# Kernel optimization log

Measured on AMD Instinct MI355X. Metric: run time of the kernel, lower is better.

The kernel has to match this reference:

```python
import jax, jax.numpy as jnp
import numpy as np

B, C, H, W = 8, 512, 64, 64
RED = 4
CR = C // RED  # 128

def setup_inputs() -> dict:
    key = jax.random.key(0)
    k1, k2, k3 = jax.random.split(key, 3)
    x = jax.random.normal(k1, (B, C, H, W), dtype=jnp.float32)
    # conv_in: 1x1 conv, no bias -> weight [3*CR, C]
    w_in = jax.random.normal(k2, (3 * CR, C), dtype=jnp.float32) * 0.02
    # conv_out: 1x1 conv, no bias -> weight [C, CR]
    w_out = jax.random.normal(k3, (C, CR), dtype=jnp.float32) * 0.02
    return {"x": x, "w_in": w_in, "w_out": w_out}

def reference(x, w_in, w_out):
    b, c, h, w = x.shape
    n = h * w
    xf = x.reshape(b, c, n)                         # flatten spatial -> [B,C,N]
    proj = jnp.einsum('oc,bcn->bon', w_in, xf)      # 1x1 conv_in -> [B,3*CR,N]
    emb_a, emb_b, g = jnp.split(proj, 3, axis=1)    # each [B,CR,N]
    # unscaled full self-attention over N spatial tokens
    weights = jnp.einsum('bcn,bcm->bnm', emb_a, emb_b)   # [B,N,N]
    weights = jax.nn.softmax(weights, axis=2)
    y = jnp.einsum('bnm,bcm->bnc', weights, g)           # [B,N,CR]
    y = jnp.einsum('oc,bnc->bon', w_out, y)              # 1x1 conv_out -> [B,C,N]
    return x + y.reshape(b, c, h, w)
```

## Files before the change

kernel.cpp:

```cpp
#include <hip/hip_runtime.h>


typedef __attribute__((ext_vector_type(8))) short short8;
typedef __attribute__((ext_vector_type(4))) float f32x4;
typedef __attribute__((ext_vector_type(16))) float f32x16;
typedef __attribute__((ext_vector_type(2))) unsigned int uint2v;

__device__ inline unsigned bfr(float f) {
  union { float f; unsigned u; } v; v.f = f;
  return v.u + 0x8000u;
}
__device__ inline unsigned short f2bf(float f) { return (unsigned short)(bfr(f) >> 16); }
__device__ inline unsigned pack2(float a, float b) {
  return __builtin_amdgcn_perm(bfr(b), bfr(a), 0x07060302u);
}
__device__ inline unsigned cvtpk(float a, float b) {
  unsigned r;
  asm("v_cvt_pk_bf16_f32 %0, %1, %2" : "=v"(r) : "v"(a), "v"(b));
  return r;
}
__device__ inline int sw(int row, int col, int stride_halves) {
  return row * stride_halves + ((((col >> 3) ^ (row & 7)) << 3) | (col & 7));
}
__device__ inline void load_lds16(const void* g, void* l) {
  __builtin_amdgcn_global_load_lds(
      (const __attribute__((address_space(1))) unsigned int*)g,
      (__attribute__((address_space(3))) unsigned int*)l, 16, 0, 0);
}

__global__ __launch_bounds__(256) void k_prep(const float* __restrict__ w_in,
                                              const float* __restrict__ w_out,
                                              unsigned short* __restrict__ wi,
                                              unsigned short* __restrict__ wo) {
  int i = blockIdx.x * 256 + threadIdx.x;
  const float* src;
  unsigned short* dst;
  int base;
  float s = 1.0f;
  if (i < 24576) {
    src = w_in;  dst = wi; base = i * 8;
    if (base < 128 * 512) s = 1.4426950408889634f;
  } else {
    src = w_out; dst = wo; base = (i - 24576) * 8;
  }
  float4 d0 = *(const float4*)&src[base];
  float4 d1 = *(const float4*)&src[base + 4];
  d0.x *= s; d0.y *= s; d0.z *= s; d0.w *= s;
  d1.x *= s; d1.y *= s; d1.z *= s; d1.w *= s;
  uint4 p;
  p.x = pack2(d0.x, d0.y); p.y = pack2(d0.z, d0.w);
  p.z = pack2(d1.x, d1.y); p.w = pack2(d1.z, d1.w);
  *(uint4*)&dst[base] = p;
}

__global__ __launch_bounds__(256, 2) void k_proj(const float* __restrict__ x,
                                                 const unsigned short* __restrict__ wi,
                                                 unsigned short* __restrict__ ab,
                                                 unsigned short* __restrict__ gC) {
  __shared__ unsigned short A_lds[384 * 64];
  __shared__ unsigned short B_lds[64 * 64];
  const int t = threadIdx.x;
  const int lane = t & 63;
  const int w = t >> 6;
  const int l15 = lane & 15;
  const int quad = lane >> 4;
  const int n0 = blockIdx.x * 64;
  const int b = blockIdx.y;
  const int ch8g = t >> 5;
  const int tp = t & 31;

  f32x4 acc[6][4];
#pragma unroll
  for (int i = 0; i < 6; i++)
#pragma unroll
    for (int j = 0; j < 4; j++) acc[i][j] = (f32x4)0.f;

  float2 d[8];
#pragma unroll
  for (int j = 0; j < 8; j++)
    d[j] = *(const float2*)&x[((size_t)(b * 512 + ch8g * 8 + j)) * 4096 + n0 + tp * 2];

  for (int k0 = 0; k0 < 512; k0 += 64) {
#pragma unroll
    for (int j = 0; j < 12; j++) {
      int row = w * 96 + j * 8 + (lane >> 3);
      int gs = (lane & 7) ^ (row & 7);
      load_lds16(&wi[(size_t)row * 512 + k0 + gs * 8],
                 (void*)&A_lds[(w * 96 + j * 8) * 64]);
    }
#pragma unroll
    for (int i = 0; i < 2; i++) {
      int r = tp * 2 + i;
      uint4 pv;
      if (i == 0) {
        pv.x = pack2(d[0].x, d[1].x); pv.y = pack2(d[2].x, d[3].x);
        pv.z = pack2(d[4].x, d[5].x); pv.w = pack2(d[6].x, d[7].x);
      } else {
        pv.x = pack2(d[0].y, d[1].y); pv.y = pack2(d[2].y, d[3].y);
        pv.z = pack2(d[4].y, d[5].y); pv.w = pack2(d[6].y, d[7].y);
      }
      *(uint4*)&B_lds[sw(r, ch8g * 8, 64)] = pv;
    }
    if (k0 + 64 < 512) {
#pragma unroll
      for (int j = 0; j < 8; j++)
        d[j] = *(const float2*)&x[((size_t)(b * 512 + k0 + 64 + ch8g * 8 + j)) * 4096 + n0 + tp * 2];
    }
    __syncthreads();
#pragma unroll
    for (int kk = 0; kk < 64; kk += 32) {
      short8 a[6];
#pragma unroll
      for (int m = 0; m < 6; m++)
        a[m] = *(const short8*)&A_lds[sw(w * 96 + m * 16 + l15, kk + quad * 8, 64)];
#pragma unroll
      for (int ns = 0; ns < 4; ns++) {
        short8 bb = *(const short8*)&B_lds[sw(ns * 16 + l15, kk + quad * 8, 64)];
#pragma unroll
        for (int m = 0; m < 6; m++)
          acc[m][ns] = __builtin_amdgcn_mfma_f32_16x16x32_bf16(a[m], bb, acc[m][ns], 0, 0, 0);
      }
    }
    __syncthreads();
  }
#pragma unroll
  for (int m = 0; m < 6; m++) {
    int o = w * 96 + m * 16 + quad * 4;
    if (o < 256) {
#pragma unroll
      for (int ns = 0; ns < 4; ns++) {
        int n = n0 + ns * 16 + l15;
        uint2 p;
        p.x = pack2(acc[m][ns][0], acc[m][ns][1]);
        p.y = pack2(acc[m][ns][2], acc[m][ns][3]);
        *(uint2*)&ab[((size_t)(b * 4096 + n)) * 256 + o] = p;
      }
    } else {
      int og = o - 256;
#pragma unroll
      for (int ns = 0; ns < 4; ns++) {
        int n = n0 + ns * 16 + l15;
#pragma unroll
        for (int r = 0; r < 4; r++)
          gC[((size_t)(b * 128 + og + r)) * 4096 + n] = f2bf(acc[m][ns][r]);
      }
    }
  }
}

__global__ __launch_bounds__(512, 2) void k_attn(const unsigned short* __restrict__ ab,
                                                 const unsigned short* __restrict__ gC,
                                                 unsigned short* __restrict__ yt) {
  __shared__ uint4 smem4[65536 / 16];
  unsigned short* smem_h = (unsigned short*)smem4;
  float* Obuf = (float*)smem4;
  float* lsumbuf = (float*)((char*)smem4 + 33024);
  unsigned* Pbuf = (unsigned*)((char*)smem4 + 33280);

  const int t = threadIdx.x;
  const int lane = t & 63;
  const int w = t >> 6;
  const int wr = w & 1;
  const int wc = w >> 1;
  const int l31 = lane & 31;
  const int h = lane >> 5;
  const int b = blockIdx.x & 7;
  const int q0 = (blockIdx.x >> 3) * 128;

  short8 qf[8];
  {
    const unsigned short* qp = &ab[((size_t)(b * 4096 + q0 + wc * 32 + l31)) * 256 + h * 8];
#pragma unroll
    for (int ks = 0; ks < 8; ks++) qf[ks] = *(const short8*)&qp[ks * 16];
  }

  auto dma_tile = [&](int kt, int buf) {
    unsigned short* Kb = smem_h + buf * 8192;
    unsigned short* Vb = smem_h + 16384 + buf * 8192;
#pragma unroll
    for (int j = 0; j < 2; j++) {
      int ck = w * 2 + j;
      int wrc = ck >> 3, ksc = ck & 7;
      load_lds16(&ab[((size_t)(b * 4096 + kt + wrc * 32 + l31)) * 256 + 128 + ksc * 16 + h * 8],
                 (void*)&Kb[ck * 512]);
    }
#pragma unroll
    for (int j = 0; j < 2; j++) {
      int cv = w * 2 + j;
      int ctc = cv >> 2, wrc = (cv >> 1) & 1, fc = cv & 1;
      load_lds16(&gC[((size_t)(b * 128 + ctc * 32 + l31)) * 4096 + kt + (wrc * 4 + fc * 2 + h) * 8],
                 (void*)&Vb[cv * 512]);
    }
  };

  f32x16 O[4];
#pragma unroll
  for (int i = 0; i < 4; i++) O[i] = (f32x16)0.f;
  float ls0 = 0.f, ls1 = 0.f, ls2 = 0.f, ls3 = 0.f;

  dma_tile(0, 0);
  __syncthreads();

  for (int it = 0; it < 64; ++it) {
    if (it < 63) dma_tile((it + 1) * 64, (it + 1) & 1);
    const unsigned short* Kc = smem_h + (it & 1) * 8192;
    const unsigned short* Vc = smem_h + 16384 + (it & 1) * 8192;

    f32x16 accS = (f32x16)0.f;
    __builtin_amdgcn_s_setprio(1);
#pragma unroll
    for (int ks = 0; ks < 8; ks++) {
      short8 ak = *(const short8*)&Kc[(wr * 8 + ks) * 512 + lane * 8];
      accS = __builtin_amdgcn_mfma_f32_32x32x16_bf16(ak, qf[ks], accS, 0, 0, 0);
    }
    __builtin_amdgcn_s_setprio(0);

    float ps[16];
#pragma unroll
    for (int r = 0; r < 16; r++) ps[r] = __builtin_amdgcn_exp2f(accS[r]);
    ls0 += ps[0] + ps[4];  ls1 += ps[1] + ps[5];
    ls2 += ps[2] + ps[6];  ls3 += ps[3] + ps[7];
    ls0 += ps[8] + ps[12]; ls1 += ps[9] + ps[13];
    ls2 += ps[10] + ps[14]; ls3 += ps[11] + ps[15];
    unsigned u[8];
#pragma unroll
    for (int i = 0; i < 8; i++) u[i] = cvtpk(ps[2 * i], ps[2 * i + 1]);

    short8 pfrag[2];
#pragma unroll
    for (int f = 0; f < 2; f++) {
      uint2v r02 = __builtin_amdgcn_permlane32_swap(u[4 * f + 0], u[4 * f + 2], false, false);
      uint2v r13 = __builtin_amdgcn_permlane32_swap(u[4 * f + 1], u[4 * f + 3], false, false);
      union { unsigned uu[4]; short8 s; } cv;
      cv.uu[0] = r02[0]; cv.uu[1] = r13[0]; cv.uu[2] = r02[1]; cv.uu[3] = r13[1];
      pfrag[f] = cv.s;
    }

    __builtin_amdgcn_s_setprio(1);
#pragma unroll
    for (int ct = 0; ct < 4; ct++) {
#pragma unroll
      for (int f = 0; f < 2; f++) {
        short8 av = *(const short8*)&Vc[(ct * 4 + wr * 2 + f) * 512 + lane * 8];
        O[ct] = __builtin_amdgcn_mfma_f32_32x32x16_bf16(av, pfrag[f], O[ct], 0, 0, 0);
      }
    }
    __builtin_amdgcn_s_setprio(0);
    __syncthreads();
  }

  float lsum = (ls0 + ls1) + (ls2 + ls3);
  lsum += __shfl_xor(lsum, 32);
#pragma unroll
  for (int p = 0; p < 2; ++p) {
    const bool act = (wc >> 1) == p;
    const int q = (wc & 1) * 32 + l31;
    if (act && wr == 0) {
#pragma unroll
      for (int ct = 0; ct < 4; ct++)
#pragma unroll
        for (int r = 0; r < 16; r++) {
          int c = ct * 32 + (r & 3) + 8 * (r >> 2) + 4 * h;
          Obuf[q * 129 + c] = O[ct][r];
        }
      if (h == 0) lsumbuf[q] = lsum;
    }
    __syncthreads();
    if (act && wr == 1) {
      float linv = 1.f / (lsum + lsumbuf[q]);
#pragma unroll
      for (int ct = 0; ct < 4; ct++)
#pragma unroll
        for (int r = 0; r < 16; r += 2) {
          int c = ct * 32 + (r & 3) + 8 * (r >> 2) + 4 * h;
          float v0 = (Obuf[q * 129 + c] + O[ct][r]) * linv;
          float v1 = (Obuf[q * 129 + c + 1] + O[ct][r + 1]) * linv;
          Pbuf[q * 65 + (c >> 1)] = pack2(v0, v1);
        }
    }
    __syncthreads();
    {
      int qq = t >> 3, seg = t & 7;
      unsigned* yrow = (unsigned*)&yt[((size_t)(b * 4096 + q0 + p * 64 + qq)) * 128];
#pragma unroll
      for (int i = 0; i < 2; i++) {
        int base = qq * 65 + seg * 8 + i * 4;
        uint4 v;
        v.x = Pbuf[base + 0];
        v.y = Pbuf[base + 1];
        v.z = Pbuf[base + 2];
        v.w = Pbuf[base + 3];
        *(uint4*)&yrow[seg * 8 + i * 4] = v;
      }
    }
  }
}

__global__ __launch_bounds__(256) void k_out(const float* __restrict__ x,
                                             const unsigned short* __restrict__ wo,
                                             const unsigned short* __restrict__ yt,
                                             float* __restrict__ out) {
  __shared__ unsigned short A_lds[128 * 128];
  __shared__ unsigned short B_lds[64 * 128];
  const int t = threadIdx.x;
  const int lane = t & 63;
  const int w = t >> 6;
  const int l15 = lane & 15;
  const int quad = lane >> 4;
  const int id = blockIdx.x;
  const int b = id & 7;
  const int rest = id >> 3;
  const int o0 = (rest & 3) * 128;
  const int n0 = (rest >> 2) * 64;

#pragma unroll
  for (int j = 0; j < 8; j++) {
    int row = w * 32 + j * 4 + (lane >> 4);
    int gs = (lane & 15) ^ (row & 7);
    load_lds16(&wo[(size_t)(o0 + row) * 128 + gs * 8],
               (void*)&A_lds[(w * 32 + j * 4) * 128]);
  }
#pragma unroll
  for (int j = 0; j < 4; j++) {
    int row = w * 16 + j * 4 + (lane >> 4);
    int gs = (lane & 15) ^ (row & 7);
    load_lds16(&yt[((size_t)(b * 4096 + n0 + row)) * 128 + gs * 8],
               (void*)&B_lds[(w * 16 + j * 4) * 128]);
  }
  __syncthreads();

  f32x4 acc[2][4];
#pragma unroll
  for (int i = 0; i < 2; i++)
#pragma unroll
    for (int j = 0; j < 4; j++) acc[i][j] = (f32x4)0.f;
#pragma unroll
  for (int ks = 0; ks < 4; ks++) {
    short8 a0 = *(const short8*)&A_lds[sw(w * 32 + l15, ks * 32 + quad * 8, 128)];
    short8 a1 = *(const short8*)&A_lds[sw(w * 32 + 16 + l15, ks * 32 + quad * 8, 128)];
#pragma unroll
    for (int ns = 0; ns < 4; ns++) {
      short8 bb = *(const short8*)&B_lds[sw(ns * 16 + l15, ks * 32 + quad * 8, 128)];
      acc[0][ns] = __builtin_amdgcn_mfma_f32_16x16x32_bf16(a0, bb, acc[0][ns], 0, 0, 0);
      acc[1][ns] = __builtin_amdgcn_mfma_f32_16x16x32_bf16(a1, bb, acc[1][ns], 0, 0, 0);
    }
  }
#pragma unroll
  for (int ms = 0; ms < 2; ms++) {
    int o = o0 + w * 32 + ms * 16 + quad * 4;
#pragma unroll
    for (int ns = 0; ns < 4; ns++) {
      int n = n0 + ns * 16 + l15;
#pragma unroll
      for (int r = 0; r < 4; r++) {
        size_t off = ((size_t)(b * 512 + o + r)) * 4096 + n;
        out[off] = x[off] + acc[ms][ns][r];
      }
    }
  }
}

extern "C" void kernel_launch(void* const* d_in, const int* in_sizes, int n_in,
                              void* d_out, int out_size, void* d_ws, size_t ws_size,
                              hipStream_t stream) {
  const float* x = (const float*)d_in[0];
  const float* w_in = (const float*)d_in[1];
  const float* w_out = (const float*)d_in[2];
  float* out = (float*)d_out;

  unsigned short* ab = (unsigned short*)d_ws;
  unsigned short* gC = ab + (size_t)8 * 4096 * 256;
  unsigned short* yt = gC + (size_t)8 * 128 * 4096;
  unsigned short* wi = yt + (size_t)8 * 4096 * 128;
  unsigned short* wo = wi + (size_t)384 * 512;

  k_prep<<<128, 256, 0, stream>>>(w_in, w_out, wi, wo);
  k_proj<<<dim3(64, 8), 256, 0, stream>>>(x, wi, ab, gC);
  k_attn<<<dim3(256), 512, 0, stream>>>(ab, gC, yt);
  k_out<<<2048, 256, 0, stream>>>(x, wo, yt, out);
}
```

Baseline: 229.4 us.

## Store K and V projections in pre-tiled LDS layout for contiguous attention loads

The projection kernel now writes Q to its own compact buffer and writes K and V directly in the per-64-key tile layout that the attention kernel's LDS staging expects. The attention tile loads become fully contiguous 8KB-per-tile copies instead of strided gathers across rows and channels. The cost is more scattered stores in the projection kernel, particularly the per-element V writes.

```diff
diff --git a/kernel.cpp b/kernel.cpp
--- a/kernel.cpp
+++ b/kernel.cpp
@@ -55,8 +55,9 @@
 
 __global__ __launch_bounds__(256, 2) void k_proj(const float* __restrict__ x,
                                                  const unsigned short* __restrict__ wi,
-                                                 unsigned short* __restrict__ ab,
-                                                 unsigned short* __restrict__ gC) {
+                                                 unsigned short* __restrict__ aq,
+                                                 unsigned short* __restrict__ Kf,
+                                                 unsigned short* __restrict__ Vf) {
   __shared__ unsigned short A_lds[384 * 64];
   __shared__ unsigned short B_lds[64 * 64];
   const int t = threadIdx.x;
@@ -64,7 +65,8 @@
   const int w = t >> 6;
   const int l15 = lane & 15;
   const int quad = lane >> 4;
-  const int n0 = blockIdx.x * 64;
+  const int tl = blockIdx.x;
+  const int n0 = tl * 64;
   const int b = blockIdx.y;
   const int ch8g = t >> 5;
   const int tp = t & 31;
@@ -123,33 +125,53 @@
     }
     __syncthreads();
   }
+  const size_t tbase = ((size_t)(b * 64 + tl)) * 8192;
 #pragma unroll
   for (int m = 0; m < 6; m++) {
     int o = w * 96 + m * 16 + quad * 4;
-    if (o < 256) {
+    if (o < 128) {
 #pragma unroll
       for (int ns = 0; ns < 4; ns++) {
         int n = n0 + ns * 16 + l15;
         uint2 p;
         p.x = pack2(acc[m][ns][0], acc[m][ns][1]);
         p.y = pack2(acc[m][ns][2], acc[m][ns][3]);
-        *(uint2*)&ab[((size_t)(b * 4096 + n)) * 256 + o] = p;
+        *(uint2*)&aq[((size_t)(b * 4096 + n)) * 128 + o] = p;
+      }
+    } else if (o < 256) {
+      int c = o - 128;
+      int ksc = c >> 4, hk = (c >> 3) & 1, e0 = c & 7;
+#pragma unroll
+      for (int ns = 0; ns < 4; ns++) {
+        int key = ns * 16 + l15;
+        int ck = (key >> 5) * 8 + ksc;
+        int lane_k = hk * 32 + (key & 31);
+        uint2 p;
+        p.x = pack2(acc[m][ns][0], acc[m][ns][1]);
+        p.y = pack2(acc[m][ns][2], acc[m][ns][3]);
+        *(uint2*)&Kf[tbase + ck * 512 + lane_k * 8 + e0] = p;
       }
     } else {
-      int og = o - 256;
+      int cb = o - 256;
 #pragma unroll
       for (int ns = 0; ns < 4; ns++) {
-        int n = n0 + ns * 16 + l15;
-#pragma unroll
-        for (int r = 0; r < 4; r++)
-          gC[((size_t)(b * 128 + og + r)) * 4096 + n] = f2bf(acc[m][ns][r]);
-      }
-    }
-  }
-}
-
-__global__ __launch_bounds__(512, 2) void k_attn(const unsigned short* __restrict__ ab,
-                                                 const unsigned short* __restrict__ gC,
+        int key = ns * 16 + l15;
+        int g8 = key >> 3;
+        int e = key & 7;
+        size_t kb = tbase + (size_t)((g8 & 1) * 32) * 8 + e + (size_t)(g8 >> 1) * 512;
+#pragma unroll
+        for (int r = 0; r < 4; r++) {
+          int c = cb + r;
+          Vf[kb + (size_t)(c >> 5) * 4 * 512 + (size_t)(c & 31) * 8] = f2bf(acc[m][ns][r]);
+        }
+      }
+    }
+  }
+}
+
+__global__ __launch_bounds__(512, 2) void k_attn(const unsigned short* __restrict__ aq,
+                                                 const unsigned short* __restrict__ Kf,
+                                                 const unsigned short* __restrict__ Vf,
                                                  unsigned short* __restrict__ yt) {
   __shared__ uint4 smem4[65536 / 16];
   unsigned short* smem_h = (unsigned short*)smem4;
@@ -169,27 +191,21 @@
 
   short8 qf[8];
   {
-    const unsigned short* qp = &ab[((size_t)(b * 4096 + q0 + wc * 32 + l31)) * 256 + h * 8];
+    const unsigned short* qp = &aq[((size_t)(b * 4096 + q0 + wc * 32 + l31)) * 128 + h * 8];
 #pragma unroll
     for (int ks = 0; ks < 8; ks++) qf[ks] = *(const short8*)&qp[ks * 16];
   }
 
-  auto dma_tile = [&](int kt, int buf) {
+  auto dma_tile = [&](int tl, int buf) {
     unsigned short* Kb = smem_h + buf * 8192;
     unsigned short* Vb = smem_h + 16384 + buf * 8192;
+    const unsigned short* Ks = &Kf[((size_t)(b * 64 + tl)) * 8192];
+    const unsigned short* Vs = &Vf[((size_t)(b * 64 + tl)) * 8192];
 #pragma unroll
     for (int j = 0; j < 2; j++) {
       int ck = w * 2 + j;
-      int wrc = ck >> 3, ksc = ck & 7;
-      load_lds16(&ab[((size_t)(b * 4096 + kt + wrc * 32 + l31)) * 256 + 128 + ksc * 16 + h * 8],
-                 (void*)&Kb[ck * 512]);
-    }
-#pragma unroll
-    for (int j = 0; j < 2; j++) {
-      int cv = w * 2 + j;
-      int ctc = cv >> 2, wrc = (cv >> 1) & 1, fc = cv & 1;
-      load_lds16(&gC[((size_t)(b * 128 + ctc * 32 + l31)) * 4096 + kt + (wrc * 4 + fc * 2 + h) * 8],
-                 (void*)&Vb[cv * 512]);
+      load_lds16(&Ks[ck * 512 + lane * 8], (void*)&Kb[ck * 512]);
+      load_lds16(&Vs[ck * 512 + lane * 8], (void*)&Vb[ck * 512]);
     }
   };
 
@@ -202,7 +218,7 @@
   __syncthreads();
 
   for (int it = 0; it < 64; ++it) {
-    if (it < 63) dma_tile((it + 1) * 64, (it + 1) & 1);
+    if (it < 63) dma_tile(it + 1, (it + 1) & 1);
     const unsigned short* Kc = smem_h + (it & 1) * 8192;
     const unsigned short* Vc = smem_h + 16384 + (it & 1) * 8192;
 
@@ -368,14 +384,15 @@
   const float* w_out = (const float*)d_in[2];
   float* out = (float*)d_out;
 
-  unsigned short* ab = (unsigned short*)d_ws;
-  unsigned short* gC = ab + (size_t)8 * 4096 * 256;
-  unsigned short* yt = gC + (size_t)8 * 128 * 4096;
+  unsigned short* aq = (unsigned short*)d_ws;
+  unsigned short* Kf = aq + (size_t)8 * 4096 * 128;
+  unsigned short* Vf = Kf + (size_t)8 * 64 * 8192;
+  unsigned short* yt = Vf + (size_t)8 * 64 * 8192;
   unsigned short* wi = yt + (size_t)8 * 4096 * 128;
   unsigned short* wo = wi + (size_t)384 * 512;
 
   k_prep<<<128, 256, 0, stream>>>(w_in, w_out, wi, wo);
-  k_proj<<<dim3(64, 8), 256, 0, stream>>>(x, wi, ab, gC);
-  k_attn<<<dim3(256), 512, 0, stream>>>(ab, gC, yt);
+  k_proj<<<dim3(64, 8), 256, 0, stream>>>(x, wi, aq, Kf, Vf);
+  k_attn<<<dim3(256), 512, 0, stream>>>(aq, Kf, Vf, yt);
   k_out<<<2048, 256, 0, stream>>>(x, wo, yt, out);
 }
```

New measurement: 215.4 us. 6.1% less time.
